# Kernel tuning notes

Hardware: AMD Instinct MI355X
Metric: run time of the kernel (lower is better)

## Reference

```python
import jax, jax.numpy as jnp
import numpy as np

EPS = 1e-6


def _dwconv3x3(x, k):
    # x: [B,C,H,W], k: [C,1,3,3] depthwise kernel (OIHW with feature_group_count=C)
    return jax.lax.conv_general_dilated(
        x, k, window_strides=(1, 1), padding='SAME',
        dimension_numbers=('NCHW', 'OIHW', 'NCHW'),
        feature_group_count=x.shape[1])


def setup_inputs() -> dict:
    key = jax.random.key(0)
    ks = jax.random.split(key, 10)
    B, C, H, W, E = 8, 128, 128, 128, 4
    s = 0.02
    return {
        'x': jax.random.normal(ks[0], (B, C, H, W), jnp.float32),
        'prompt': jax.random.normal(ks[1], (B, C), jnp.float32),
        'gamma': jnp.ones((C,), jnp.float32),
        'beta': jnp.zeros((C,), jnp.float32),
        'rw': jax.random.normal(ks[2], (2 * C, E), jnp.float32) * s,
        'rb': jnp.zeros((E,), jnp.float32),
        'w1': jax.random.normal(ks[3], (E, C, C), jnp.float32) * s,
        'b1': jnp.zeros((E, C), jnp.float32),
        'dw': jax.random.normal(ks[4], (E, C, 1, 3, 3), jnp.float32) * s,
        'bdw': jnp.zeros((E, C), jnp.float32),
        'w2': jax.random.normal(ks[5], (E, C, C), jnp.float32) * s,
        'b2': jnp.zeros((E, C), jnp.float32),
        'pw': jax.random.normal(ks[6], (C, C), jnp.float32) * s,
        'pb': jnp.zeros((C,), jnp.float32),
    }


def reference(x, prompt, gamma, beta, rw, rb, w1, b1, dw, bdw, w2, b2, pw, pb):
    B, C, H, W = x.shape
    E = rb.shape[0]
    topk = 2

    # LayerNorm over channel dim (applied on last axis after permute in torch)
    mu = x.mean(axis=1, keepdims=True)
    var = x.var(axis=1, keepdims=True)
    x_in = (x - mu) * jax.lax.rsqrt(var + EPS)
    x_in = x_in * gamma[None, :, None, None] + beta[None, :, None, None]

    # Router: global avg pooled feature + prompt -> softmax -> top-k
    feat_avg = x_in.mean(axis=(2, 3))                        # [B,C]
    logits = jnp.concatenate([feat_avg, prompt], axis=1) @ rw + rb  # [B,E]
    probs = jax.nn.softmax(logits, axis=-1)
    weights, indices = jax.lax.top_k(probs, topk)            # [B,topk]

    # Per-sample gate over experts: g[b,e] = sum_k weights[b,k] * (indices[b,k]==e)
    gate = jnp.einsum('bk,bke->be', weights, jax.nn.one_hot(indices, E, dtype=x.dtype))

    # Dense all-expert compute (as in the original masked implementation)
    y = jnp.einsum('bchw,eoc->ebohw', x_in, w1) + b1[:, None, :, None, None]  # [E,B,C,H,W]
    y = jax.vmap(_dwconv3x3, in_axes=(0, 0))(y, dw) + bdw[:, None, :, None, None]
    y = jax.nn.gelu(y, approximate=False)
    y = jnp.einsum('ebchw,eoc->ebohw', y, w2) + b2[:, None, :, None, None]

    out = jnp.einsum('ebchw,be->bchw', y, gate)
    proj = jnp.einsum('bchw,oc->bohw', out, pw) + pb[None, :, None, None]
    return x + proj
```

## Files before the change

kernel.cpp:

```cpp
#include <hip/hip_runtime.h>
#include <hip/hip_bf16.h>

#define BB 8
#define CC 128
#define HH 128
#define WW 128
#define HW (HH*WW)
#define EE 4
#define EPSL 1e-6f
#define PT1 8
#define PT2 4
#define LNP 128

typedef __attribute__((ext_vector_type(8))) short bf16x8;
typedef __attribute__((ext_vector_type(4))) float f32x4;

__device__ inline float b2f(unsigned short u){
  union { unsigned int i; float f; } v; v.i = ((unsigned int)u)<<16; return v.f;
}
__device__ inline unsigned short f2b(float f){
  union { float f; unsigned int i; } v; v.f = f;
  unsigned int x = v.i;
  return (unsigned short)((x + 0x7fffu + ((x>>16)&1u)) >> 16);
}

__global__ __launch_bounds__(128) void k_ln(
    const float* __restrict__ x, const float* __restrict__ gamma,
    const float* __restrict__ beta, unsigned short* __restrict__ xin,
    float* __restrict__ feat_sum) {
  int b = blockIdx.y;
  int p0 = blockIdx.x*LNP;
  int tid = threadIdx.x;
  const float* xb = x + (size_t)b*CC*HW + p0 + tid;
  float s=0.f, s2=0.f;
  for (int c=0;c<CC;c++){ float v = xb[(size_t)c*HW]; s+=v; s2+=v*v; }
  float mu = s*(1.f/CC);
  float var = s2*(1.f/CC) - mu*mu;
  float rs = rsqrtf(var + EPSL);

  __shared__ unsigned short tile[LNP][CC+8];
  __shared__ float lfeat[CC];
  for (int c=tid;c<CC;c+=LNP) lfeat[c]=0.f;
  __syncthreads();

  int lane = tid & 63;
  for (int c0=0;c0<CC;c0+=8){
    union { bf16x8 v; unsigned short s[8]; } pk;
    float vs[8];
    #pragma unroll
    for (int j=0;j<8;j++){
      float v = (xb[(size_t)(c0+j)*HW]-mu)*rs*gamma[c0+j]+beta[c0+j];
      vs[j]=v; pk.s[j]=f2b(v);
    }
    *(bf16x8*)&tile[tid][c0] = pk.v;
    #pragma unroll
    for (int j=0;j<8;j++){
      float r = vs[j];
      for (int o=32;o>0;o>>=1) r += __shfl_down(r, o);
      if (lane==0) atomicAdd(&lfeat[c0+j], r);
    }
  }
  __syncthreads();

  unsigned short* xo = xin + ((size_t)b*HW + p0)*CC;
  #pragma unroll
  for (int it=0; it<LNP*CC/(LNP*8); ++it){
    int i = it*LNP + tid;
    int pr = i>>4, ck = (i&15)*8;
    *(bf16x8*)(xo + (size_t)i*8) = *(bf16x8*)&tile[pr][ck];
  }
  for (int c=tid;c<CC;c+=LNP) atomicAdd(&feat_sum[b*CC+c], lfeat[c]);
}

__global__ __launch_bounds__(256) void k_router(
    const float* __restrict__ feat_sum, const float* __restrict__ prompt,
    const float* __restrict__ rw, const float* __restrict__ rb,
    const float* __restrict__ b2, const float* __restrict__ pw,
    const float* __restrict__ pb,
    int* __restrict__ eidx, float* __restrict__ wgt, float* __restrict__ bias_out) {
  __shared__ float logits[BB][EE];
  __shared__ float gate[BB][EE];
  __shared__ float cb[BB][CC];
  int t = threadIdx.x;
  if (t < BB*EE) {
    int b = t/EE, e = t%EE;
    float acc = rb[e];
    for (int c=0;c<CC;c++) acc += (feat_sum[b*CC+c]*(1.f/HW))*rw[c*EE+e];
    for (int c=0;c<CC;c++) acc += prompt[b*CC+c]*rw[(CC+c)*EE+e];
    logits[b][e]=acc;
  }
  __syncthreads();
  if (t < BB) {
    int b=t;
    float m=-1e30f;
    for(int e=0;e<EE;e++) m=fmaxf(m,logits[b][e]);
    float s=0.f, pr[EE];
    for(int e=0;e<EE;e++){ pr[e]=__expf(logits[b][e]-m); s+=pr[e]; }
    for(int e=0;e<EE;e++){ pr[e]/=s; gate[b][e]=0.f; }
    int i1=0; for(int e=1;e<EE;e++) if (pr[e]>pr[i1]) i1=e;
    int i2=-1; for(int e=0;e<EE;e++){ if(e==i1) continue; if(i2<0||pr[e]>pr[i2]) i2=e; }
    eidx[b*2]=i1; eidx[b*2+1]=i2;
    wgt[b*2]=pr[i1]; wgt[b*2+1]=pr[i2];
    gate[b][i1]=pr[i1]; gate[b][i2]=pr[i2];
  }
  __syncthreads();
  for (int i=t;i<BB*CC;i+=256){
    int b=i/CC, c=i%CC;
    float a=0.f;
    for(int e=0;e<EE;e++) a += gate[b][e]*b2[e*CC+c];
    cb[b][c]=a;
  }
  __syncthreads();
  for (int i=t;i<BB*CC;i+=256){
    int b=i/CC, o=i%CC;
    float a=pb[o];
    for (int c=0;c<CC;c++) a += pw[o*CC+c]*cb[b][c];
    bias_out[b*CC+o]=a;
  }
}

__global__ __launch_bounds__(128) void k_prep(
    const float* __restrict__ pw, const float* __restrict__ w2,
    const float* __restrict__ w1,
    unsigned short* __restrict__ w2p, unsigned short* __restrict__ w1b){
  int eo = blockIdx.x; int e = eo/CC, o = eo%CC;
  int c = threadIdx.x;
  float a=0.f;
  for (int m=0;m<CC;m++) a += pw[o*CC+m]*w2[((size_t)e*CC+m)*CC+c];
  w2p[((size_t)e*CC+o)*CC+c] = f2b(a);
  w1b[((size_t)e*CC+o)*CC+c] = f2b(w1[((size_t)e*CC+o)*CC+c]);
}

__global__ __launch_bounds__(256) void k_scalew2(
    const unsigned short* __restrict__ w2p, const int* __restrict__ eidx,
    const float* __restrict__ wgt, unsigned short* __restrict__ w2s){
  int bk = blockIdx.y;
  int e = eidx[bk]; float wv = wgt[bk];
  int i = blockIdx.x*256 + threadIdx.x;
  const unsigned short* src = w2p + (size_t)e*CC*CC;
  w2s[(size_t)bk*CC*CC + i] = f2b(wv * b2f(src[i]));
}

__global__ __launch_bounds__(256) void k_gemm1(
    const unsigned short* __restrict__ xin, const unsigned short* __restrict__ w1b,
    const float* __restrict__ b1, const int* __restrict__ eidx,
    unsigned short* __restrict__ t1) {
  int bk = blockIdx.y; int b = bk>>1; int e = eidx[bk];
  int wave = threadIdx.x>>6, lane = threadIdx.x&63;
  int lr = lane&15, lg = lane>>4;
  int ob = wave*32;
  const unsigned short* Ae = w1b + (size_t)e*CC*CC;
  bf16x8 A[2][4];
  #pragma unroll
  for (int of=0; of<2; of++)
    #pragma unroll
    for (int k0=0; k0<4; k0++)
      A[of][k0] = *(const bf16x8*)(Ae + (size_t)(ob+of*16+lr)*CC + k0*32 + lg*8);
  float bs[2][4];
  #pragma unroll
  for (int of=0; of<2; of++)
    #pragma unroll
    for (int r=0; r<4; r++)
      bs[of][r] = b1[e*CC + ob + of*16 + lg*4 + r];

  int p_start = blockIdx.x * (32*PT1);
  const unsigned short* Xb = xin + ((size_t)b*HW + p_start)*CC;
  unsigned short* T = t1 + ((size_t)bk*HW + p_start)*CC;

  bf16x8 Ba[2][4], Bb[2][4];
  auto loadB = [&](bf16x8 (&Bf)[2][4], int tt){
    const unsigned short* Xt = Xb + (size_t)tt*32*CC;
    #pragma unroll
    for (int pf=0; pf<2; pf++)
      #pragma unroll
      for (int k0=0; k0<4; k0++)
        Bf[pf][k0] = *(const bf16x8*)(Xt + (size_t)(pf*16+lr)*CC + k0*32 + lg*8);
  };
  auto comp = [&](bf16x8 (&Bf)[2][4], int tt){
    f32x4 acc[2][2];
    #pragma unroll
    for (int of=0; of<2; of++){ acc[of][0]=(f32x4){0,0,0,0}; acc[of][1]=(f32x4){0,0,0,0}; }
    #pragma unroll
    for (int k0=0; k0<4; k0++)
      #pragma unroll
      for (int of=0; of<2; of++)
        #pragma unroll
        for (int pf=0; pf<2; pf++)
          acc[of][pf] = __builtin_amdgcn_mfma_f32_16x16x32_bf16(A[of][k0], Bf[pf][k0], acc[of][pf],0,0,0);
    unsigned short* Tt = T + (size_t)tt*32*CC;
    #pragma unroll
    for (int of=0; of<2; of++){
      int o0 = ob + of*16 + lg*4;
      #pragma unroll
      for (int pf=0; pf<2; pf++){
        union { unsigned long long u; unsigned short s[4]; } pk;
        #pragma unroll
        for (int r=0; r<4; r++) pk.s[r]=f2b(acc[of][pf][r]+bs[of][r]);
        *(unsigned long long*)(Tt + (size_t)(pf*16+lr)*CC + o0) = pk.u;
      }
    }
  };

  loadB(Ba, 0);
  #pragma unroll
  for (int t=0; t<PT1; t++){
    if ((t&1)==0){ if (t+1<PT1) loadB(Bb, t+1); comp(Ba, t); }
    else         { if (t+1<PT1) loadB(Ba, t+1); comp(Bb, t); }
  }
}

__global__ __launch_bounds__(256) void k_dw(
    const unsigned short* __restrict__ t1, const float* __restrict__ dw,
    const float* __restrict__ bdw, const int* __restrict__ eidx,
    unsigned short* __restrict__ t3) {
  int bk = blockIdx.y; int e = eidx[bk];
  int h  = blockIdx.x;
  int cg = (threadIdx.x & 15) * 8;
  int ws = (threadIdx.x >> 4) * 8;

  __shared__ float skd[CC*9];
  __shared__ float sbd[CC];
  {
    const float* src = dw + (size_t)e*CC*9;
    for (int i=threadIdx.x; i<CC*9; i+=256) skd[i] = src[i];
    for (int i=threadIdx.x; i<CC;   i+=256) sbd[i] = bdw[e*CC+i];
  }
  __syncthreads();

  float acc[8][8];
  #pragma unroll
  for (int px=0; px<8; px++)
    #pragma unroll
    for (int j=0; j<8; j++) acc[px][j] = sbd[cg+j];

  const unsigned short* rowbase = t1 + ((size_t)bk*HW + (size_t)h*WW)*CC + cg;

  #pragma unroll
  for (int dy=0; dy<3; dy++){
    int h2 = h + dy - 1;
    if (h2 < 0 || h2 >= HH) continue;
    const unsigned short* rp = rowbase + (size_t)(dy-1)*WW*CC;
    bf16x8 v[10];
    #pragma unroll
    for (int t=0; t<10; t++){
      int wc = ws + t - 1;
      if (wc >= 0 && wc < WW) v[t] = *(const bf16x8*)(rp + (size_t)wc*CC);
      else                    v[t] = (bf16x8){0,0,0,0,0,0,0,0};
    }
    #pragma unroll
    for (int dx=0; dx<3; dx++){
      float wk[8];
      #pragma unroll
      for (int j=0; j<8; j++) wk[j] = skd[(cg+j)*9 + dy*3 + dx];
      #pragma unroll
      for (int px=0; px<8; px++){
        #pragma unroll
        for (int j=0; j<8; j++)
          acc[px][j] += b2f((unsigned short)v[px+dx][j]) * wk[j];
      }
    }
  }

  unsigned short* dst = t3 + ((size_t)bk*HW + (size_t)h*WW + ws)*CC + cg;
  #pragma unroll
  for (int px=0; px<8; px++){
    union { bf16x8 v; unsigned short s[8]; } pk;
    #pragma unroll
    for (int j=0; j<8; j++){
      float a = acc[px][j];
      float g = 0.5f*a*(1.f+erff(a*0.70710678f));
      pk.s[j] = f2b(g);
    }
    *(bf16x8*)(dst + (size_t)px*CC) = pk.v;
  }
}

__global__ __launch_bounds__(256) void k_gemm2(
    const unsigned short* __restrict__ t3, const unsigned short* __restrict__ w2s,
    const float* __restrict__ bias_out, const float* __restrict__ x,
    float* __restrict__ out) {
  int b = blockIdx.y;
  int wave = threadIdx.x>>6, lane = threadIdx.x&63;
  int lr = lane&15, lg = lane>>4;
  int ob = wave*32;
  bf16x8 A[2][2][4];
  #pragma unroll
  for (int kk=0; kk<2; kk++){
    const unsigned short* Ae = w2s + (size_t)(b*2+kk)*CC*CC;
    #pragma unroll
    for (int of=0; of<2; of++)
      #pragma unroll
      for (int k0=0; k0<4; k0++)
        A[kk][of][k0] = *(const bf16x8*)(Ae + (size_t)(ob+of*16+lr)*CC + k0*32 + lg*8);
  }
  float bo[2][4];
  #pragma unroll
  for (int of=0; of<2; of++)
    #pragma unroll
    for (int r=0; r<4; r++)
      bo[of][r] = bias_out[b*CC + ob + of*16 + lg*4 + r];

  int p_start = blockIdx.x * (32*PT2);
  const unsigned short* X0 = t3 + ((size_t)(b*2+0)*HW + p_start)*CC;
  const unsigned short* X1 = t3 + ((size_t)(b*2+1)*HW + p_start)*CC;
  const float* xb = x + (size_t)b*CC*HW;
  float* obp = out + (size_t)b*CC*HW;

  bf16x8 Ba[2][4], Bb[2][4];
  auto loadB = [&](bf16x8 (&Bf)[2][4], int g){
    const unsigned short* Xt = ((g&1) ? X1 : X0) + (size_t)(g>>1)*32*CC;
    #pragma unroll
    for (int pf=0; pf<2; pf++)
      #pragma unroll
      for (int k0=0; k0<4; k0++)
        Bf[pf][k0] = *(const bf16x8*)(Xt + (size_t)(pf*16+lr)*CC + k0*32 + lg*8);
  };

  f32x4 acc[2][2];
  auto comp = [&](bf16x8 (&Bf)[2][4], int g){
    int kk = g&1, tt = g>>1;
    if (kk==0){
      #pragma unroll
      for (int of=0; of<2; of++){ acc[of][0]=(f32x4){0,0,0,0}; acc[of][1]=(f32x4){0,0,0,0}; }
    }
    #pragma unroll
    for (int k0=0; k0<4; k0++)
      #pragma unroll
      for (int of=0; of<2; of++)
        #pragma unroll
        for (int pf=0; pf<2; pf++)
          acc[of][pf] = (kk==0)
            ? __builtin_amdgcn_mfma_f32_16x16x32_bf16(A[0][of][k0], Bf[pf][k0], acc[of][pf],0,0,0)
            : __builtin_amdgcn_mfma_f32_16x16x32_bf16(A[1][of][k0], Bf[pf][k0], acc[of][pf],0,0,0);
    if (kk==1){
      #pragma unroll
      for (int of=0; of<2; of++){
        int o0 = ob + of*16 + lg*4;
        #pragma unroll
        for (int r=0; r<4; r++){
          #pragma unroll
          for (int pf=0; pf<2; pf++){
            size_t idx = (size_t)(o0+r)*HW + p_start + tt*32 + pf*16 + lr;
            obp[idx] = xb[idx] + acc[of][pf][r] + bo[of][r];
          }
        }
      }
    }
  };

  loadB(Ba, 0);
  #pragma unroll
  for (int g=0; g<2*PT2; g++){
    if ((g&1)==0){ if (g+1<2*PT2) loadB(Bb, g+1); comp(Ba, g); }
    else         { if (g+1<2*PT2) loadB(Ba, g+1); comp(Bb, g); }
  }
}

extern "C" void kernel_launch(void* const* d_in, const int* in_sizes, int n_in,
                              void* d_out, int out_size, void* d_ws, size_t ws_size,
                              hipStream_t stream) {
  const float* x      = (const float*)d_in[0];
  const float* prompt = (const float*)d_in[1];
  const float* gamma  = (const float*)d_in[2];
  const float* beta   = (const float*)d_in[3];
  const float* rw     = (const float*)d_in[4];
  const float* rb     = (const float*)d_in[5];
  const float* w1     = (const float*)d_in[6];
  const float* b1     = (const float*)d_in[7];
  const float* dw     = (const float*)d_in[8];
  const float* bdw    = (const float*)d_in[9];
  const float* w2     = (const float*)d_in[10];
  const float* b2     = (const float*)d_in[11];
  const float* pw     = (const float*)d_in[12];
  const float* pb     = (const float*)d_in[13];
  float* out = (float*)d_out;

  char* base = (char*)d_ws;
  size_t off = 0;
  auto alloc = [&](size_t bytes)->void* {
    void* p = base + off;
    off = (off + bytes + 255) & ~(size_t)255;
    return p;
  };
  unsigned short* xin  = (unsigned short*)alloc((size_t)BB*HW*CC*2);
  unsigned short* t1   = (unsigned short*)alloc((size_t)BB*2*HW*CC*2);
  unsigned short* t3   = (unsigned short*)alloc((size_t)BB*2*HW*CC*2);
  unsigned short* w1b  = (unsigned short*)alloc((size_t)EE*CC*CC*2);
  unsigned short* w2p  = (unsigned short*)alloc((size_t)EE*CC*CC*2);
  unsigned short* w2s  = (unsigned short*)alloc((size_t)BB*2*CC*CC*2);
  float* feat_sum      = (float*)alloc(BB*CC*4);
  int*   eidx          = (int*)alloc(BB*2*4);
  float* wgt           = (float*)alloc(BB*2*4);
  float* bias_out      = (float*)alloc(BB*CC*4);

  hipMemsetAsync(feat_sum, 0, BB*CC*4, stream);

  k_ln<<<dim3(HW/LNP, BB), LNP, 0, stream>>>(x, gamma, beta, xin, feat_sum);
  k_prep<<<dim3(EE*CC), 128, 0, stream>>>(pw, w2, w1, w2p, w1b);
  k_router<<<dim3(1), 256, 0, stream>>>(feat_sum, prompt, rw, rb, b2, pw, pb,
                                        eidx, wgt, bias_out);
  k_scalew2<<<dim3(CC*CC/256, BB*2), 256, 0, stream>>>(w2p, eidx, wgt, w2s);
  k_gemm1<<<dim3(HW/(32*PT1), BB*2), 256, 0, stream>>>(xin, w1b, b1, eidx, t1);
  k_dw<<<dim3(HH, BB*2), 256, 0, stream>>>(t1, dw, bdw, eidx, t3);
  k_gemm2<<<dim3(HW/(32*PT2), BB), 256, 0, stream>>>(t3, w2s, bias_out, x, out);
}
```

Before: 358.6 us.

## Fuse depthwise conv+GELU with second GEMM through LDS; split feature pooling from LN

The depthwise 3x3 conv and GELU now write their output row into a swizzled shared-memory tile, which the second MFMA GEMM reads directly. This removes the global t3 intermediate and its full write and read-back. The channel-mean reduction for the router also moves out of the LayerNorm kernel into a separate kernel that re-reads the bf16 normalized activations, so LN no longer does wave shuffles and LDS atomics. In exchange, the fused kernel uses about 74KB of LDS with a smaller grid, which lowers occupancy. The router average is now computed from bf16-rounded values.

```diff
diff --git a/kernel.cpp b/kernel.cpp
--- a/kernel.cpp
+++ b/kernel.cpp
@@ -9,7 +9,6 @@
 #define EE 4
 #define EPSL 1e-6f
 #define PT1 8
-#define PT2 4
 #define LNP 128
 
 typedef __attribute__((ext_vector_type(8))) short bf16x8;
@@ -23,11 +22,13 @@
   unsigned int x = v.i;
   return (unsigned short)((x + 0x7fffu + ((x>>16)&1u)) >> 16);
 }
+__device__ inline int swz(int px, int cbyte){
+  return cbyte ^ ((((px)&7) ^ (((px)>>3)&3)) << 4);
+}
 
 __global__ __launch_bounds__(128) void k_ln(
     const float* __restrict__ x, const float* __restrict__ gamma,
-    const float* __restrict__ beta, unsigned short* __restrict__ xin,
-    float* __restrict__ feat_sum) {
+    const float* __restrict__ beta, unsigned short* __restrict__ xin) {
   int b = blockIdx.y;
   int p0 = blockIdx.x*LNP;
   int tid = threadIdx.x;
@@ -39,37 +40,47 @@
   float rs = rsqrtf(var + EPSL);
 
   __shared__ unsigned short tile[LNP][CC+8];
-  __shared__ float lfeat[CC];
-  for (int c=tid;c<CC;c+=LNP) lfeat[c]=0.f;
-  __syncthreads();
-
-  int lane = tid & 63;
   for (int c0=0;c0<CC;c0+=8){
     union { bf16x8 v; unsigned short s[8]; } pk;
-    float vs[8];
     #pragma unroll
     for (int j=0;j<8;j++){
       float v = (xb[(size_t)(c0+j)*HW]-mu)*rs*gamma[c0+j]+beta[c0+j];
-      vs[j]=v; pk.s[j]=f2b(v);
+      pk.s[j]=f2b(v);
     }
     *(bf16x8*)&tile[tid][c0] = pk.v;
-    #pragma unroll
-    for (int j=0;j<8;j++){
-      float r = vs[j];
-      for (int o=32;o>0;o>>=1) r += __shfl_down(r, o);
-      if (lane==0) atomicAdd(&lfeat[c0+j], r);
-    }
-  }
-  __syncthreads();
-
+  }
+  __syncthreads();
   unsigned short* xo = xin + ((size_t)b*HW + p0)*CC;
   #pragma unroll
-  for (int it=0; it<LNP*CC/(LNP*8); ++it){
+  for (int it=0; it<16; ++it){
     int i = it*LNP + tid;
     int pr = i>>4, ck = (i&15)*8;
     *(bf16x8*)(xo + (size_t)i*8) = *(bf16x8*)&tile[pr][ck];
   }
-  for (int c=tid;c<CC;c+=LNP) atomicAdd(&feat_sum[b*CC+c], lfeat[c]);
+}
+
+__global__ __launch_bounds__(256) void k_feat(
+    const unsigned short* __restrict__ xin, float* __restrict__ feat_sum) {
+  int b = blockIdx.y;
+  int g = blockIdx.x;
+  int tid = threadIdx.x;
+  int cg = (tid & 15) * 8;
+  int po = tid >> 4;
+  __shared__ float lfeat[CC];
+  for (int c=tid;c<CC;c+=256) lfeat[c]=0.f;
+  __syncthreads();
+  const unsigned short* base = xin + ((size_t)b*HW + (size_t)g*128)*CC + cg;
+  float acc[8] = {};
+  #pragma unroll
+  for (int i=0;i<8;i++){
+    bf16x8 v = *(const bf16x8*)(base + (size_t)(i*16+po)*CC);
+    #pragma unroll
+    for (int j=0;j<8;j++) acc[j] += b2f((unsigned short)v[j]);
+  }
+  #pragma unroll
+  for (int j=0;j<8;j++) atomicAdd(&lfeat[cg+j], acc[j]);
+  __syncthreads();
+  if (tid < CC) atomicAdd(&feat_sum[b*CC+tid], lfeat[tid]);
 }
 
 __global__ __launch_bounds__(256) void k_router(
@@ -209,78 +220,82 @@
   }
 }
 
-__global__ __launch_bounds__(256) void k_dw(
+__global__ __launch_bounds__(256) void k_dwg2(
     const unsigned short* __restrict__ t1, const float* __restrict__ dw,
     const float* __restrict__ bdw, const int* __restrict__ eidx,
-    unsigned short* __restrict__ t3) {
-  int bk = blockIdx.y; int e = eidx[bk];
-  int h  = blockIdx.x;
-  int cg = (threadIdx.x & 15) * 8;
-  int ws = (threadIdx.x >> 4) * 8;
-
-  __shared__ float skd[CC*9];
-  __shared__ float sbd[CC];
-  {
-    const float* src = dw + (size_t)e*CC*9;
-    for (int i=threadIdx.x; i<CC*9; i+=256) skd[i] = src[i];
-    for (int i=threadIdx.x; i<CC;   i+=256) sbd[i] = bdw[e*CC+i];
-  }
-  __syncthreads();
-
-  float acc[8][8];
-  #pragma unroll
-  for (int px=0; px<8; px++)
-    #pragma unroll
-    for (int j=0; j<8; j++) acc[px][j] = sbd[cg+j];
-
-  const unsigned short* rowbase = t1 + ((size_t)bk*HW + (size_t)h*WW)*CC + cg;
-
-  #pragma unroll
-  for (int dy=0; dy<3; dy++){
-    int h2 = h + dy - 1;
-    if (h2 < 0 || h2 >= HH) continue;
-    const unsigned short* rp = rowbase + (size_t)(dy-1)*WW*CC;
-    bf16x8 v[10];
-    #pragma unroll
-    for (int t=0; t<10; t++){
-      int wc = ws + t - 1;
-      if (wc >= 0 && wc < WW) v[t] = *(const bf16x8*)(rp + (size_t)wc*CC);
-      else                    v[t] = (bf16x8){0,0,0,0,0,0,0,0};
-    }
-    #pragma unroll
-    for (int dx=0; dx<3; dx++){
-      float wk[8];
-      #pragma unroll
-      for (int j=0; j<8; j++) wk[j] = skd[(cg+j)*9 + dy*3 + dx];
-      #pragma unroll
-      for (int px=0; px<8; px++){
-        #pragma unroll
-        for (int j=0; j<8; j++)
-          acc[px][j] += b2f((unsigned short)v[px+dx][j]) * wk[j];
-      }
-    }
-  }
-
-  unsigned short* dst = t3 + ((size_t)bk*HW + (size_t)h*WW + ws)*CC + cg;
-  #pragma unroll
-  for (int px=0; px<8; px++){
-    union { bf16x8 v; unsigned short s[8]; } pk;
-    #pragma unroll
-    for (int j=0; j<8; j++){
-      float a = acc[px][j];
-      float g = 0.5f*a*(1.f+erff(a*0.70710678f));
-      pk.s[j] = f2b(g);
-    }
-    *(bf16x8*)(dst + (size_t)px*CC) = pk.v;
-  }
-}
-
-__global__ __launch_bounds__(256) void k_gemm2(
-    const unsigned short* __restrict__ t3, const unsigned short* __restrict__ w2s,
-    const float* __restrict__ bias_out, const float* __restrict__ x,
-    float* __restrict__ out) {
+    const unsigned short* __restrict__ w2s, const float* __restrict__ bias_out,
+    const float* __restrict__ x, float* __restrict__ out) {
   int b = blockIdx.y;
-  int wave = threadIdx.x>>6, lane = threadIdx.x&63;
+  int h = blockIdx.x;
+  int tid = threadIdx.x;
+
+  __shared__ unsigned short t3s[2][HH*CC/HH*CC/CC];
+  __shared__ unsigned short tile2[2][128*CC];
+  __shared__ float skd2[2][CC*9];
+  __shared__ float sbd2[2][CC];
+  (void)t3s;
+
+  int e0 = eidx[b*2], e1 = eidx[b*2+1];
+  for (int i=tid; i<2*CC*9; i+=256){
+    int kk = i/(CC*9), j = i%(CC*9);
+    skd2[kk][j] = dw[(size_t)(kk? e1:e0)*CC*9 + j];
+  }
+  for (int i=tid; i<2*CC; i+=256){
+    int kk = i/CC, j = i%CC;
+    sbd2[kk][j] = bdw[(kk? e1:e0)*CC + j];
+  }
+  __syncthreads();
+
+  int cg = (tid & 15) * 8;
+  int ws = (tid >> 4) * 8;
+
+  #pragma unroll
+  for (int kk=0; kk<2; kk++){
+    float acc[8][8];
+    #pragma unroll
+    for (int px=0; px<8; px++)
+      #pragma unroll
+      for (int j=0; j<8; j++) acc[px][j] = sbd2[kk][cg+j];
+
+    const unsigned short* rowbase = t1 + ((size_t)(b*2+kk)*HW + (size_t)h*WW)*CC + cg;
+    #pragma unroll
+    for (int dy=0; dy<3; dy++){
+      int h2 = h + dy - 1;
+      if (h2 < 0 || h2 >= HH) continue;
+      const unsigned short* rp = rowbase + (size_t)(dy-1)*WW*CC;
+      bf16x8 v[10];
+      #pragma unroll
+      for (int t=0; t<10; t++){
+        int wc = ws + t - 1;
+        if (wc >= 0 && wc < WW) v[t] = *(const bf16x8*)(rp + (size_t)wc*CC);
+        else                    v[t] = (bf16x8){0,0,0,0,0,0,0,0};
+      }
+      #pragma unroll
+      for (int dx=0; dx<3; dx++){
+        float wk[8];
+        #pragma unroll
+        for (int j=0; j<8; j++) wk[j] = skd2[kk][(cg+j)*9 + dy*3 + dx];
+        #pragma unroll
+        for (int px=0; px<8; px++)
+          #pragma unroll
+          for (int j=0; j<8; j++)
+            acc[px][j] += b2f((unsigned short)v[px+dx][j]) * wk[j];
+      }
+    }
+    #pragma unroll
+    for (int px=0; px<8; px++){
+      union { bf16x8 v; unsigned short s[8]; } pk;
+      #pragma unroll
+      for (int j=0; j<8; j++){
+        float a = acc[px][j];
+        pk.s[j] = f2b(0.5f*a*(1.f+erff(a*0.70710678f)));
+      }
+      int p = ws + px;
+      *(bf16x8*)((char*)&tile2[kk][0] + p*256 + swz(p, cg*2)) = pk.v;
+    }
+  }
+
+  int wave = tid>>6, lane = tid&63;
   int lr = lane&15, lg = lane>>4;
   int ob = wave*32;
   bf16x8 A[2][2][4];
@@ -300,59 +315,42 @@
     for (int r=0; r<4; r++)
       bo[of][r] = bias_out[b*CC + ob + of*16 + lg*4 + r];
 
-  int p_start = blockIdx.x * (32*PT2);
-  const unsigned short* X0 = t3 + ((size_t)(b*2+0)*HW + p_start)*CC;
-  const unsigned short* X1 = t3 + ((size_t)(b*2+1)*HW + p_start)*CC;
-  const float* xb = x + (size_t)b*CC*HW;
-  float* obp = out + (size_t)b*CC*HW;
-
-  bf16x8 Ba[2][4], Bb[2][4];
-  auto loadB = [&](bf16x8 (&Bf)[2][4], int g){
-    const unsigned short* Xt = ((g&1) ? X1 : X0) + (size_t)(g>>1)*32*CC;
-    #pragma unroll
-    for (int pf=0; pf<2; pf++)
-      #pragma unroll
-      for (int k0=0; k0<4; k0++)
-        Bf[pf][k0] = *(const bf16x8*)(Xt + (size_t)(pf*16+lr)*CC + k0*32 + lg*8);
-  };
-
-  f32x4 acc[2][2];
-  auto comp = [&](bf16x8 (&Bf)[2][4], int g){
-    int kk = g&1, tt = g>>1;
-    if (kk==0){
-      #pragma unroll
-      for (int of=0; of<2; of++){ acc[of][0]=(f32x4){0,0,0,0}; acc[of][1]=(f32x4){0,0,0,0}; }
-    }
-    #pragma unroll
-    for (int k0=0; k0<4; k0++)
-      #pragma unroll
-      for (int of=0; of<2; of++)
-        #pragma unroll
-        for (int pf=0; pf<2; pf++)
-          acc[of][pf] = (kk==0)
-            ? __builtin_amdgcn_mfma_f32_16x16x32_bf16(A[0][of][k0], Bf[pf][k0], acc[of][pf],0,0,0)
-            : __builtin_amdgcn_mfma_f32_16x16x32_bf16(A[1][of][k0], Bf[pf][k0], acc[of][pf],0,0,0);
-    if (kk==1){
-      #pragma unroll
-      for (int of=0; of<2; of++){
-        int o0 = ob + of*16 + lg*4;
-        #pragma unroll
-        for (int r=0; r<4; r++){
-          #pragma unroll
-          for (int pf=0; pf<2; pf++){
-            size_t idx = (size_t)(o0+r)*HW + p_start + tt*32 + pf*16 + lr;
-            obp[idx] = xb[idx] + acc[of][pf][r] + bo[of][r];
-          }
+  __syncthreads();
+
+  const float* xb = x + (size_t)b*CC*HW + (size_t)h*WW;
+  float* obp = out + (size_t)b*CC*HW + (size_t)h*WW;
+
+  #pragma unroll
+  for (int tt=0; tt<4; tt++){
+    f32x4 acc[2][2];
+    #pragma unroll
+    for (int of=0; of<2; of++){ acc[of][0]=(f32x4){0,0,0,0}; acc[of][1]=(f32x4){0,0,0,0}; }
+    #pragma unroll
+    for (int kk=0; kk<2; kk++){
+      #pragma unroll
+      for (int k0=0; k0<4; k0++){
+        int cb = k0*64 + lg*16;
+        bf16x8 B0 = *(bf16x8*)((char*)&tile2[kk][0] + (tt*32+lr   )*256 + swz(tt*32+lr,    cb));
+        bf16x8 B1 = *(bf16x8*)((char*)&tile2[kk][0] + (tt*32+16+lr)*256 + swz(tt*32+16+lr, cb));
+        #pragma unroll
+        for (int of=0; of<2; of++){
+          acc[of][0] = __builtin_amdgcn_mfma_f32_16x16x32_bf16(A[kk][of][k0], B0, acc[of][0],0,0,0);
+          acc[of][1] = __builtin_amdgcn_mfma_f32_16x16x32_bf16(A[kk][of][k0], B1, acc[of][1],0,0,0);
         }
       }
     }
-  };
-
-  loadB(Ba, 0);
-  #pragma unroll
-  for (int g=0; g<2*PT2; g++){
-    if ((g&1)==0){ if (g+1<2*PT2) loadB(Bb, g+1); comp(Ba, g); }
-    else         { if (g+1<2*PT2) loadB(Ba, g+1); comp(Bb, g); }
+    #pragma unroll
+    for (int of=0; of<2; of++){
+      int o0 = ob + of*16 + lg*4;
+      #pragma unroll
+      for (int r=0; r<4; r++){
+        #pragma unroll
+        for (int pf=0; pf<2; pf++){
+          size_t idx = (size_t)(o0+r)*HW + tt*32 + pf*16 + lr;
+          obp[idx] = xb[idx] + acc[of][pf][r] + bo[of][r];
+        }
+      }
+    }
   }
 }
 
@@ -384,7 +382,6 @@
   };
   unsigned short* xin  = (unsigned short*)alloc((size_t)BB*HW*CC*2);
   unsigned short* t1   = (unsigned short*)alloc((size_t)BB*2*HW*CC*2);
-  unsigned short* t3   = (unsigned short*)alloc((size_t)BB*2*HW*CC*2);
   unsigned short* w1b  = (unsigned short*)alloc((size_t)EE*CC*CC*2);
   unsigned short* w2p  = (unsigned short*)alloc((size_t)EE*CC*CC*2);
   unsigned short* w2s  = (unsigned short*)alloc((size_t)BB*2*CC*CC*2);
@@ -395,12 +392,12 @@
 
   hipMemsetAsync(feat_sum, 0, BB*CC*4, stream);
 
-  k_ln<<<dim3(HW/LNP, BB), LNP, 0, stream>>>(x, gamma, beta, xin, feat_sum);
+  k_ln<<<dim3(HW/LNP, BB), LNP, 0, stream>>>(x, gamma, beta, xin);
+  k_feat<<<dim3(128, BB), 256, 0, stream>>>(xin, feat_sum);
   k_prep<<<dim3(EE*CC), 128, 0, stream>>>(pw, w2, w1, w2p, w1b);
   k_router<<<dim3(1), 256, 0, stream>>>(feat_sum, prompt, rw, rb, b2, pw, pb,
                                         eidx, wgt, bias_out);
   k_scalew2<<<dim3(CC*CC/256, BB*2), 256, 0, stream>>>(w2p, eidx, wgt, w2s);
   k_gemm1<<<dim3(HW/(32*PT1), BB*2), 256, 0, stream>>>(xin, w1b, b1, eidx, t1);
-  k_dw<<<dim3(HH, BB*2), 256, 0, stream>>>(t1, dw, bdw, eidx, t3);
-  k_gemm2<<<dim3(HW/(32*PT2), BB), 256, 0, stream>>>(t3, w2s, bias_out, x, out);
-}
+  k_dwg2<<<dim3(HH, BB), 256, 0, stream>>>(t1, dw, bdw, eidx, w2s, bias_out, x, out);
+}
```

Result: faster. 326.5 us (-8.9%).
